# Kernel optimization log

Measured on AMD Instinct MI355X. Metric: run time of the kernel, lower is better.

Reference implementation:

```python
import jax, jax.numpy as jnp
import numpy as np

B, S, D, H, DFF = 2, 2048, 2048, 16, 8192
DH = D // H
EPS = 1e-5


def _layer_norm(x, g, b):
    mu = jnp.mean(x, axis=-1, keepdims=True)
    var = jnp.mean(jnp.square(x - mu), axis=-1, keepdims=True)
    return (x - mu) * jax.lax.rsqrt(var + EPS) * g + b


def setup_inputs() -> dict:
    key = jax.random.key(0)
    ks = jax.random.split(key, 12)
    sc = 0.02
    inp = {
        "x": jax.random.normal(ks[0], (B, S, D), dtype=jnp.float32),
        # attention projections, stored [in, out] (torch Linear weight transposed)
        "wq": jax.random.normal(ks[1], (D, D), dtype=jnp.float32) * sc,
        "bq": jnp.zeros((D,), jnp.float32),
        "wk": jax.random.normal(ks[2], (D, D), dtype=jnp.float32) * sc,
        "bk": jnp.zeros((D,), jnp.float32),
        "wv": jax.random.normal(ks[3], (D, D), dtype=jnp.float32) * sc,
        "bv": jnp.zeros((D,), jnp.float32),
        "wo": jax.random.normal(ks[4], (D, D), dtype=jnp.float32) * sc,
        "bo": jnp.zeros((D,), jnp.float32),
        "ln1_g": jnp.ones((D,), jnp.float32),
        "ln1_b": jnp.zeros((D,), jnp.float32),
        # feed-forward
        "w1": jax.random.normal(ks[5], (D, DFF), dtype=jnp.float32) * sc,
        "b1": jnp.zeros((DFF,), jnp.float32),
        "w2": jax.random.normal(ks[6], (DFF, D), dtype=jnp.float32) * sc,
        "b2": jnp.zeros((D,), jnp.float32),
        "ln2_g": jnp.ones((D,), jnp.float32),
        "ln2_b": jnp.zeros((D,), jnp.float32),
    }
    return inp


def reference(x, wq, bq, wk, bk, wv, bv, wo, bo, ln1_g, ln1_b,
              w1, b1, w2, b2, ln2_g, ln2_b):
    # ---- MultiHeadAttentionBlock: x + MHA(LN(x)) ----
    h = _layer_norm(x, ln1_g, ln1_b)                      # [B,S,D]
    q = (h @ wq + bq).reshape(B, S, H, DH).transpose(0, 2, 1, 3)  # [B,H,S,DH]
    k = (h @ wk + bk).reshape(B, S, H, DH).transpose(0, 2, 1, 3)
    v = (h @ wv + bv).reshape(B, S, H, DH).transpose(0, 2, 1, 3)

    # faithful to source: scale by sqrt(d_dim), NOT sqrt(head_dim)
    scores = jnp.einsum("bhqd,bhkd->bhqk", q, k) / np.sqrt(D).astype(np.float32)
    # faithful triu/transpose masking (softmax sees raw zeros, not -inf)
    t = jnp.triu(scores).swapaxes(-2, -1)                 # [B,H,S,S]
    s = jax.nn.softmax(t, axis=-2)
    r = jnp.triu(s).swapaxes(-2, -1)
    attn = jnp.einsum("bhqk,bhkd->bhqd", r, v)            # [B,H,S,DH]
    attn = attn.transpose(0, 2, 1, 3).reshape(B, S, D)
    x = x + attn @ wo + bo

    # ---- FeedForwardBlock: x + FF(LN(x)), dropout rate 0 ----
    h2 = _layer_norm(x, ln2_g, ln2_b)
    ff = jax.nn.relu(h2 @ w1 + b1) @ w2 + b2
    return x + ff
```

## Files before the change

### kernel.cpp

```cpp
#include <hip/hip_runtime.h>


typedef unsigned short ushort_t;
typedef unsigned int   uint32;
typedef __attribute__((ext_vector_type(8)))  short    short8;
typedef __attribute__((ext_vector_type(8)))  ushort_t ushort8;
typedef __attribute__((ext_vector_type(4)))  float    f32x4;

#define BDIM   2
#define SEQ    2048
#define DMODEL 2048
#define NHEAD  16
#define DHEAD  128
#define DFFN   8192
#define MROWS  (BDIM*SEQ)
#define LDQKV  6144

#define GPTR(p) (const __attribute__((address_space(1))) void*)((const void*)(p))
#define SPTR(p) (__attribute__((address_space(3))) void*)((void*)(p))

__device__ __forceinline__ float bf2f(ushort_t u) {
  union { uint32 i; float f; } c; c.i = ((uint32)u) << 16; return c.f;
}
__device__ __forceinline__ ushort_t f2bf(float f) {
  union { float f; uint32 i; } c; c.f = f;
  uint32 u = c.i;
  return (ushort_t)((u + 0x7fffu + ((u >> 16) & 1u)) >> 16);
}

__global__ __launch_bounds__(256) void prep_kern(
    const float* __restrict__ wq, const float* __restrict__ wk,
    const float* __restrict__ wv, const float* __restrict__ wo,
    const float* __restrict__ w1, const float* __restrict__ w2,
    const float* __restrict__ bq, const float* __restrict__ bk,
    const float* __restrict__ bv,
    ushort_t* __restrict__ WQKV, ushort_t* __restrict__ WOT,
    ushort_t* __restrict__ W1T, ushort_t* __restrict__ W2T,
    float* __restrict__ Bcat)
{
  const int bid = blockIdx.x;
  if (bid >= 49152) {
    for (int i = threadIdx.x; i < 6144; i += 256)
      Bcat[i] = (i < 2048) ? bq[i] : ((i < 4096) ? bk[i - 2048] : bv[i - 4096]);
    return;
  }
  const float* W; ushort_t* Wt; int K, N, local;
  if (bid < 12288) {
    const int which = bid >> 12; local = bid & 4095;
    W = (which == 0) ? wq : (which == 1) ? wk : wv;
    Wt = WQKV + (size_t)which * 2048 * 2048; K = 2048; N = 2048;
  } else if (bid < 16384) { W = wo; Wt = WOT; K = 2048; N = 2048; local = bid - 12288; }
  else if (bid < 32768)   { W = w1; Wt = W1T; K = 2048; N = 8192; local = bid - 16384; }
  else                    { W = w2; Wt = W2T; K = 8192; N = 2048; local = bid - 32768; }
  const int ntiles = N >> 5;
  const int nb = (local % ntiles) * 32, kb = (local / ntiles) * 32;

  __shared__ float tile[32][33];
  const int tx = threadIdx.x & 31, ty = threadIdx.x >> 5;
#pragma unroll
  for (int j = 0; j < 32; j += 8)
    tile[ty + j][tx] = W[(size_t)(kb + ty + j) * N + nb + tx];
  __syncthreads();
#pragma unroll
  for (int j = 0; j < 32; j += 8)
    Wt[(size_t)(nb + ty + j) * K + kb + tx] = f2bf(tile[tx][ty + j]);
}

__global__ __launch_bounds__(256) void ln_kern(
    const float* __restrict__ X, const float* __restrict__ G,
    const float* __restrict__ Bb, ushort_t* __restrict__ Out)
{
  const int row = blockIdx.x, tid = threadIdx.x;
  const float* xr = X + (size_t)row * DMODEL;
  float4 v0 = ((const float4*)xr)[tid * 2];
  float4 v1 = ((const float4*)xr)[tid * 2 + 1];
  float s  = v0.x + v0.y + v0.z + v0.w + v1.x + v1.y + v1.z + v1.w;
  float ss = v0.x*v0.x + v0.y*v0.y + v0.z*v0.z + v0.w*v0.w
           + v1.x*v1.x + v1.y*v1.y + v1.z*v1.z + v1.w*v1.w;
#pragma unroll
  for (int off = 32; off > 0; off >>= 1) {
    s  += __shfl_down(s, off);
    ss += __shfl_down(ss, off);
  }
  __shared__ float rs[4], rss[4];
  __shared__ float sh_mu, sh_rst;
  const int wv = tid >> 6;
  if ((tid & 63) == 0) { rs[wv] = s; rss[wv] = ss; }
  __syncthreads();
  if (tid == 0) {
    float S1 = rs[0] + rs[1] + rs[2] + rs[3];
    float S2 = rss[0] + rss[1] + rss[2] + rss[3];
    float mu = S1 * (1.f / DMODEL);
    float var = S2 * (1.f / DMODEL) - mu * mu;
    sh_mu = mu;
    sh_rst = rsqrtf(var + 1e-5f);
  }
  __syncthreads();
  const float mu = sh_mu, rst = sh_rst;
  float4 g0 = ((const float4*)G)[tid * 2];
  float4 g1 = ((const float4*)G)[tid * 2 + 1];
  float4 b0 = ((const float4*)Bb)[tid * 2];
  float4 b1 = ((const float4*)Bb)[tid * 2 + 1];
  ushort8 o;
  o[0] = f2bf((v0.x - mu) * rst * g0.x + b0.x);
  o[1] = f2bf((v0.y - mu) * rst * g0.y + b0.y);
  o[2] = f2bf((v0.z - mu) * rst * g0.z + b0.z);
  o[3] = f2bf((v0.w - mu) * rst * g0.w + b0.w);
  o[4] = f2bf((v1.x - mu) * rst * g1.x + b1.x);
  o[5] = f2bf((v1.y - mu) * rst * g1.y + b1.y);
  o[6] = f2bf((v1.z - mu) * rst * g1.z + b1.z);
  o[7] = f2bf((v1.w - mu) * rst * g1.w + b1.w);
  *(ushort8*)(Out + (size_t)row * DMODEL + tid * 8) = o;
}

__global__ __launch_bounds__(256) void combine_ln_kern(
    const ushort_t* __restrict__ pp, const float* __restrict__ bias,
    const float* __restrict__ xres, const float* __restrict__ G,
    const float* __restrict__ Bb, float* __restrict__ X2,
    ushort_t* __restrict__ Out)
{
  const int row = blockIdx.x, tid = threadIdx.x;
  const size_t i = (size_t)row * DMODEL + tid * 8;
  ushort8 p0 = *(const ushort8*)(pp + i);
  ushort8 p1 = *(const ushort8*)(pp + (size_t)MROWS * 2048 + i);
  float v[8];
#pragma unroll
  for (int j = 0; j < 8; ++j)
    v[j] = bf2f(p0[j]) + bf2f(p1[j]) + bias[tid * 8 + j] + xres[i + j];
  float4 o0 = {v[0], v[1], v[2], v[3]}, o1 = {v[4], v[5], v[6], v[7]};
  *(float4*)(X2 + i) = o0;
  *(float4*)(X2 + i + 4) = o1;

  float s = 0.f, ss = 0.f;
#pragma unroll
  for (int j = 0; j < 8; ++j) { s += v[j]; ss += v[j] * v[j]; }
#pragma unroll
  for (int off = 32; off > 0; off >>= 1) {
    s  += __shfl_down(s, off);
    ss += __shfl_down(ss, off);
  }
  __shared__ float rs[4], rss[4];
  __shared__ float sh_mu, sh_rst;
  const int wvv = tid >> 6;
  if ((tid & 63) == 0) { rs[wvv] = s; rss[wvv] = ss; }
  __syncthreads();
  if (tid == 0) {
    float S1 = rs[0] + rs[1] + rs[2] + rs[3];
    float S2 = rss[0] + rss[1] + rss[2] + rss[3];
    float mu = S1 * (1.f / DMODEL);
    float var = S2 * (1.f / DMODEL) - mu * mu;
    sh_mu = mu; sh_rst = rsqrtf(var + 1e-5f);
  }
  __syncthreads();
  const float mu = sh_mu, rst = sh_rst;
  ushort8 o;
#pragma unroll
  for (int j = 0; j < 8; ++j)
    o[j] = f2bf((v[j] - mu) * rst * G[tid * 8 + j] + Bb[tid * 8 + j]);
  *(ushort8*)(Out + i) = o;
}

template<int OUT, int RELU, int KDIV>
__global__ __launch_bounds__(512) void gemm_hi_kern(
    const ushort_t* __restrict__ A, const ushort_t* __restrict__ Bt,
    const float* __restrict__ bias, ushort_t* __restrict__ Cout,
    int M, int N, int K)
{
  __shared__ ushort_t sA[3 * 4096];
  __shared__ ushort_t sB[3 * 8192];

  const int tid = threadIdx.x;
  const int nM  = gridDim.y;
  const int nwg = gridDim.x * nM;
  const int bid = blockIdx.y * gridDim.x + blockIdx.x;
  const int cpx = nwg >> 3;
  const int swz = (bid & 7) * cpx + (bid >> 3);
  const int m0 = (swz % nM) * 128;
  const int n0 = (swz / nM) * 256;

  const int Keff = K / KDIV;
  const int k0 = (KDIV > 1) ? blockIdx.z * Keff : 0;
  const int U = Keff >> 5;

  const int l = tid & 63, w = tid >> 6;
  const int lr = l & 15, lg = l >> 4;
  const int wr = w >> 2, wc = w & 3;

  const int xch   = (lg ^ ((lr >> 1) & 3)) * 8;
  const int abase = (wr * 64 + lr) * 32 + xch;
  const int bbase = (wc * 64 + lr) * 32 + xch;

  const int sr = tid >> 2;
  const int sg = ((tid & 3) ^ ((tid >> 3) & 3)) * 8;
  const ushort_t* Asrc = A  + (size_t)(m0 + sr) * K + k0 + sg;
  const ushort_t* Bsrc = Bt + (size_t)(n0 + sr) * K + k0 + sg;
  ushort_t* dA = sA + tid * 8;
  ushort_t* dB = sB + tid * 8;

#define SAU(slot, u) __builtin_amdgcn_global_load_lds( \
    GPTR(Asrc + (size_t)(u) * 32), SPTR(dA + (slot) * 4096), 16, 0, 0)
#define SBU(slot, u, r) __builtin_amdgcn_global_load_lds( \
    GPTR(Bsrc + (size_t)(r) * 128 * K + (size_t)(u) * 32), \
    SPTR(dB + (slot) * 8192 + (r) * 4096), 16, 0, 0)

  f32x4 acc[4][4] = {};

  SAU(0, 0); SBU(0, 0, 0); SBU(0, 0, 1);
  SAU(1, 1); SBU(1, 1, 0); SBU(1, 1, 1);
  asm volatile("s_waitcnt vmcnt(3)" ::: "memory");
  __builtin_amdgcn_s_barrier();

  int cur = 0;
  for (int u = 0; u < U; ++u) {
    const ushort_t* pA = sA + cur * 4096;
    const ushort_t* pB = sB + cur * 8192;
    const int nx = (cur == 0) ? 2 : cur - 1;
    short8 af[4], bf[4];
#pragma unroll
    for (int i = 0; i < 4; ++i) af[i] = *(const short8*)(pA + abase + i * 512);
#pragma unroll
    for (int i = 0; i < 4; ++i) bf[i] = *(const short8*)(pB + bbase + i * 512);
    if (u + 2 < U) { SAU(nx, u + 2); SBU(nx, u + 2, 0); SBU(nx, u + 2, 1); }
    __builtin_amdgcn_s_setprio(1);
#pragma unroll
    for (int mi = 0; mi < 4; ++mi)
#pragma unroll
      for (int ni = 0; ni < 4; ++ni)
        acc[mi][ni] = __builtin_amdgcn_mfma_f32_16x16x32_bf16(
            af[mi], bf[ni], acc[mi][ni], 0, 0, 0);
    __builtin_amdgcn_s_setprio(0);
    if (u < U - 2) { asm volatile("s_waitcnt vmcnt(3)" ::: "memory"); }
    else           { asm volatile("s_waitcnt vmcnt(0)" ::: "memory"); }
    __builtin_amdgcn_s_barrier();
    cur = (cur == 2) ? 0 : cur + 1;
  }
#undef SAU
#undef SBU

  ushort_t* Pz = (OUT == 2)
      ? Cout + (size_t)blockIdx.z * M * N : Cout;
#pragma unroll
  for (int mi = 0; mi < 4; ++mi) {
#pragma unroll
    for (int ni = 0; ni < 4; ++ni) {
      const int gn = n0 + wc * 64 + ni * 16 + lr;
      const float bvv = (OUT == 2) ? 0.f : bias[gn];
#pragma unroll
      for (int j = 0; j < 4; ++j) {
        const int gm = m0 + wr * 64 + mi * 16 + lg * 4 + j;
        float v = acc[mi][ni][j] + bvv;
        if (RELU) v = fmaxf(v, 0.f);
        Pz[(size_t)gm * N + gn] = f2bf(v);
      }
    }
  }
}

__global__ __launch_bounds__(256) void combine_kern(
    const ushort_t* __restrict__ pp, const float* __restrict__ bias,
    const float* __restrict__ resid, float* __restrict__ out)
{
  const size_t i = ((size_t)blockIdx.x * 256 + threadIdx.x) * 8;
  ushort8 p0 = *(const ushort8*)(pp + i);
  ushort8 p1 = *(const ushort8*)(pp + (size_t)MROWS * 2048 + i);
  const int col = (int)(i & 2047);
  float4 r0 = *(const float4*)(resid + i);
  float4 r1 = *(const float4*)(resid + i + 4);
  float4 c0 = *(const float4*)(bias + col);
  float4 c1 = *(const float4*)(bias + col + 4);
  float4 o0, o1;
  o0.x = bf2f(p0[0]) + bf2f(p1[0]) + c0.x + r0.x;
  o0.y = bf2f(p0[1]) + bf2f(p1[1]) + c0.y + r0.y;
  o0.z = bf2f(p0[2]) + bf2f(p1[2]) + c0.z + r0.z;
  o0.w = bf2f(p0[3]) + bf2f(p1[3]) + c0.w + r0.w;
  o1.x = bf2f(p0[4]) + bf2f(p1[4]) + c1.x + r1.x;
  o1.y = bf2f(p0[5]) + bf2f(p1[5]) + c1.y + r1.y;
  o1.z = bf2f(p0[6]) + bf2f(p1[6]) + c1.z + r1.z;
  o1.w = bf2f(p0[7]) + bf2f(p1[7]) + c1.w + r1.w;
  *(float4*)(out + i) = o0;
  *(float4*)(out + i + 4) = o1;
}

__global__ __launch_bounds__(256) void attn_stats_kern(
    const ushort_t* __restrict__ Q, const ushort_t* __restrict__ Kb,
    float* __restrict__ E, float* __restrict__ DG, int ld)
{
  __shared__ ushort_t Ksm[2 * 8192];
  const int qb = blockIdx.x;
  const int bh = blockIdx.y;
  const int b = bh >> 4, h = bh & 15;
  const int tid = threadIdx.x;
  const int l = tid & 63, w = tid >> 6;
  const int lr = l & 15, lg = l >> 4;

  const int qrow0 = qb * 128 + w * 32;

  short8 af[2][4];
#pragma unroll
  for (int g = 0; g < 2; ++g) {
    const size_t qoff = (size_t)(b * SEQ + qrow0 + g * 16 + lr) * ld + h * DHEAD + lg * 8;
#pragma unroll
    for (int c = 0; c < 4; ++c) af[g][c] = *(const short8*)(Q + qoff + c * 32);
  }

  const int srow_b = w * 16 + (l >> 4);
  const ushort_t* Kg = Kb + (size_t)b * SEQ * ld + (size_t)h * DHEAD;

  f32x4 sume[2] = {{0.f,0.f,0.f,0.f},{0.f,0.f,0.f,0.f}};
  f32x4 dge[2]  = {{0.f,0.f,0.f,0.f},{0.f,0.f,0.f,0.f}};
  const float scale = 0.0220970869120796f;
  const int rx = lr & 7;
  const int kc0 = qb * 2;

#define STAGEK(kc, buf) do { \
    _Pragma("unroll") \
    for (int c_ = 0; c_ < 4; ++c_) { \
      const int row_ = srow_b + c_ * 4; \
      const int g_ = (l & 15) ^ (row_ & 7); \
      __builtin_amdgcn_global_load_lds( \
          GPTR(Kg + (size_t)((kc) * 64 + row_) * ld + g_ * 8), \
          SPTR(Ksm + (buf) * 8192 + w * 2048 + c_ * 512), 16, 0, 0); \
    } } while (0)

  STAGEK(kc0, 0);
  __syncthreads();

  int cur = 0;
  for (int kc = kc0; kc < 32; ++kc) {
    if (kc + 1 < 32) STAGEK(kc + 1, cur ^ 1);
    const ushort_t* Kbuf = Ksm + cur * 8192;

    for (int ks = 0; ks < 4; ++ks) {
      const int kbase = kc * 64 + ks * 16;
      if (kbase + 16 <= qrow0) continue;
      short8 bfr[4];
#pragma unroll
      for (int c = 0; c < 4; ++c)
        bfr[c] = *(const short8*)(Kbuf + (ks * 16 + lr) * 128 + ((lg + c * 4) ^ rx) * 8);
#pragma unroll
      for (int g = 0; g < 2; ++g) {
        const int qg = qrow0 + g * 16;
        if (kbase < qg) continue;
        f32x4 sc = {0.f, 0.f, 0.f, 0.f};
        sc = __builtin_amdgcn_mfma_f32_16x16x32_bf16(af[g][0], bfr[0], sc, 0, 0, 0);
        sc = __builtin_amdgcn_mfma_f32_16x16x32_bf16(af[g][1], bfr[1], sc, 0, 0, 0);
        sc = __builtin_amdgcn_mfma_f32_16x16x32_bf16(af[g][2], bfr[2], sc, 0, 0, 0);
        sc = __builtin_amdgcn_mfma_f32_16x16x32_bf16(af[g][3], bfr[3], sc, 0, 0, 0);
        if (kbase == qg) {
          const int ki = kbase + lr;
#pragma unroll
          for (int j = 0; j < 4; ++j) {
            const int qi = qg + lg * 4 + j;
            if (ki >= qi) {
              float e = __expf(sc[j] * scale);
              sume[g][j] += e;
              if (ki == qi) dge[g][j] += e;
            }
          }
        } else {
#pragma unroll
          for (int j = 0; j < 4; ++j)
            sume[g][j] += __expf(sc[j] * scale);
        }
      }
    }
    __syncthreads();
    cur ^= 1;
  }
#undef STAGEK

#pragma unroll
  for (int g = 0; g < 2; ++g) {
#pragma unroll
    for (int j = 0; j < 4; ++j) {
#pragma unroll
      for (int off = 1; off < 16; off <<= 1) {
        sume[g][j] += __shfl_xor(sume[g][j], off);
        dge[g][j]  += __shfl_xor(dge[g][j], off);
      }
    }
  }
  if (lr == 0) {
#pragma unroll
    for (int g = 0; g < 2; ++g)
#pragma unroll
      for (int j = 0; j < 4; ++j) {
        E[(size_t)bh * SEQ + qrow0 + g * 16 + lg * 4 + j]  = sume[g][j];
        DG[(size_t)bh * SEQ + qrow0 + g * 16 + lg * 4 + j] = dge[g][j];
      }
  }
}

__global__ __launch_bounds__(128) void vchunk_kern(
    const ushort_t* __restrict__ V, float* __restrict__ CS, int ld)
{
  const int c = blockIdx.x, bh = blockIdx.y;
  const int b = bh >> 4, h = bh & 15;
  const int dh = threadIdx.x;
  const ushort_t* vp = V + (size_t)(b * SEQ + c * 64) * ld + h * DHEAD + dh;
  float s = 0.f;
  for (int i = 0; i < 64; ++i) s += bf2f(vp[(size_t)i * ld]);
  CS[((size_t)bh * 32 + c) * 128 + dh] = s;
}

__global__ __launch_bounds__(128) void attn_combine_kern(
    const ushort_t* __restrict__ V, const float* __restrict__ CS,
    const float* __restrict__ E, const float* __restrict__ DG,
    ushort_t* __restrict__ Attn, int ldv)
{
  const int c = blockIdx.x, bh = blockIdx.y;
  const int b = bh >> 4, h = bh & 15;
  const int dh = threadIdx.x;
  float prefix = 0.f;
  for (int cc = 0; cc < c; ++cc) prefix += CS[((size_t)bh * 32 + cc) * 128 + dh];
  const ushort_t* vp = V + (size_t)(b * SEQ + c * 64) * ldv + h * DHEAD + dh;
  ushort_t* ap = Attn + (size_t)(b * SEQ + c * 64) * DMODEL + h * DHEAD + dh;
  const int qb = c * 64;
  for (int i = 0; i < 64; ++i) {
    const int qq = qb + i;
    const float denom = (float)qq + E[(size_t)bh * SEQ + qq];
    const float de = DG[(size_t)bh * SEQ + qq];
    const float vv = bf2f(vp[(size_t)i * ldv]);
    ap[(size_t)i * DMODEL] = f2bf((prefix + de * vv) / denom);
    prefix += vv;
  }
}

extern "C" void kernel_launch(void* const* d_in, const int* in_sizes, int n_in,
                              void* d_out, int out_size, void* d_ws, size_t ws_size,
                              hipStream_t stream)
{
  const float* x    = (const float*)d_in[0];
  const float* wq   = (const float*)d_in[1];
  const float* bq   = (const float*)d_in[2];
  const float* wk   = (const float*)d_in[3];
  const float* bk   = (const float*)d_in[4];
  const float* wv   = (const float*)d_in[5];
  const float* bv   = (const float*)d_in[6];
  const float* wo   = (const float*)d_in[7];
  const float* bo   = (const float*)d_in[8];
  const float* ln1g = (const float*)d_in[9];
  const float* ln1b = (const float*)d_in[10];
  const float* w1   = (const float*)d_in[11];
  const float* b1   = (const float*)d_in[12];
  const float* w2   = (const float*)d_in[13];
  const float* b2   = (const float*)d_in[14];
  const float* ln2g = (const float*)d_in[15];
  const float* ln2b = (const float*)d_in[16];
  float* out = (float*)d_out;

  char* ws = (char*)d_ws;
  ushort_t* W1T  = (ushort_t*)(ws + 0);
  ushort_t* PPf2 = (ushort_t*)(ws + 0);
  ushort_t* W2T  = (ushort_t*)(ws + 33554432);
  ushort_t* WOT  = (ushort_t*)(ws + 67108864);
  float*    X2   = (float*)   (ws + 75497472);
  float*    Bcat = (float*)   (ws + 75497472);
  ushort_t* Hb   = (ushort_t*)(ws + 109051904);
  ushort_t* F1   = (ushort_t*)(ws + 125829120);
  ushort_t* PPwo = (ushort_t*)(ws + 125829120);
  ushort_t* WQKV = (ushort_t*)(ws + 125829120);
  ushort_t* QKVb = (ushort_t*)(ws + 150994944);
  float*    Eb   = (float*)   (ws + 201326592);
  float*    DGb  = (float*)   (ws + 201588736);
  float*    CSb  = (float*)   (ws + 201850880);

  prep_kern<<<49153, 256, 0, stream>>>(wq, wk, wv, wo, w1, w2, bq, bk, bv,
                                       WQKV, WOT, W1T, W2T, Bcat);

  ln_kern<<<MROWS, 256, 0, stream>>>(x, ln1g, ln1b, Hb);

  gemm_hi_kern<1, 0, 1><<<dim3(24, 32), 512, 0, stream>>>(
      Hb, WQKV, Bcat, QKVb, MROWS, LDQKV, DMODEL);

  attn_stats_kern<<<dim3(16, 32), 256, 0, stream>>>(QKVb, QKVb + 2048, Eb, DGb, LDQKV);

  vchunk_kern<<<dim3(32, 32), 128, 0, stream>>>(QKVb + 4096, CSb, LDQKV);
  attn_combine_kern<<<dim3(32, 32), 128, 0, stream>>>(QKVb + 4096, CSb, Eb, DGb, Hb, LDQKV);

  gemm_hi_kern<2, 0, 2><<<dim3(8, 32, 2), 512, 0, stream>>>(
      Hb, WOT, bo, PPwo, MROWS, DMODEL, DMODEL);

  combine_ln_kern<<<MROWS, 256, 0, stream>>>(PPwo, bo, x, ln2g, ln2b, X2, Hb);

  gemm_hi_kern<1, 1, 1><<<dim3(32, 32), 512, 0, stream>>>(
      Hb, W1T, b1, F1, MROWS, DFFN, DMODEL);

  gemm_hi_kern<2, 0, 2><<<dim3(8, 32, 2), 512, 0, stream>>>(
      F1, W2T, b2, PPf2, MROWS, DMODEL, DFFN);
  combine_kern<<<4096, 256, 0, stream>>>(PPf2, b2, X2, out);
}
```

Measured before the change: 619.9 us.

## Drop split-K for output GEMMs and fuse bias plus residual into epilogue

The Wo and W2 projections no longer use split-K with bf16 partial buffers followed by separate combine kernels. The GEMM epilogue now adds bias and the fp32 residual and writes fp32 output directly, and the second LayerNorm reuses the plain ln_kern on X2. This removes two extra kernels, the partial-sum traffic, and a bf16 rounding of the partials. In exchange those GEMMs launch only 256 workgroups instead of 512, which lowers occupancy on a large-CU GPU, and the epilogue issues scattered 4-byte fp32 stores.

```diff
diff --git a/kernel.cpp b/kernel.cpp
--- a/kernel.cpp
+++ b/kernel.cpp
@@ -113,58 +113,11 @@
   *(ushort8*)(Out + (size_t)row * DMODEL + tid * 8) = o;
 }
 
-__global__ __launch_bounds__(256) void combine_ln_kern(
-    const ushort_t* __restrict__ pp, const float* __restrict__ bias,
-    const float* __restrict__ xres, const float* __restrict__ G,
-    const float* __restrict__ Bb, float* __restrict__ X2,
-    ushort_t* __restrict__ Out)
-{
-  const int row = blockIdx.x, tid = threadIdx.x;
-  const size_t i = (size_t)row * DMODEL + tid * 8;
-  ushort8 p0 = *(const ushort8*)(pp + i);
-  ushort8 p1 = *(const ushort8*)(pp + (size_t)MROWS * 2048 + i);
-  float v[8];
-#pragma unroll
-  for (int j = 0; j < 8; ++j)
-    v[j] = bf2f(p0[j]) + bf2f(p1[j]) + bias[tid * 8 + j] + xres[i + j];
-  float4 o0 = {v[0], v[1], v[2], v[3]}, o1 = {v[4], v[5], v[6], v[7]};
-  *(float4*)(X2 + i) = o0;
-  *(float4*)(X2 + i + 4) = o1;
-
-  float s = 0.f, ss = 0.f;
-#pragma unroll
-  for (int j = 0; j < 8; ++j) { s += v[j]; ss += v[j] * v[j]; }
-#pragma unroll
-  for (int off = 32; off > 0; off >>= 1) {
-    s  += __shfl_down(s, off);
-    ss += __shfl_down(ss, off);
-  }
-  __shared__ float rs[4], rss[4];
-  __shared__ float sh_mu, sh_rst;
-  const int wvv = tid >> 6;
-  if ((tid & 63) == 0) { rs[wvv] = s; rss[wvv] = ss; }
-  __syncthreads();
-  if (tid == 0) {
-    float S1 = rs[0] + rs[1] + rs[2] + rs[3];
-    float S2 = rss[0] + rss[1] + rss[2] + rss[3];
-    float mu = S1 * (1.f / DMODEL);
-    float var = S2 * (1.f / DMODEL) - mu * mu;
-    sh_mu = mu; sh_rst = rsqrtf(var + 1e-5f);
-  }
-  __syncthreads();
-  const float mu = sh_mu, rst = sh_rst;
-  ushort8 o;
-#pragma unroll
-  for (int j = 0; j < 8; ++j)
-    o[j] = f2bf((v[j] - mu) * rst * G[tid * 8 + j] + Bb[tid * 8 + j]);
-  *(ushort8*)(Out + i) = o;
-}
-
-template<int OUT, int RELU, int KDIV>
+template<int OUT, int RELU>
 __global__ __launch_bounds__(512) void gemm_hi_kern(
     const ushort_t* __restrict__ A, const ushort_t* __restrict__ Bt,
-    const float* __restrict__ bias, ushort_t* __restrict__ Cout,
-    int M, int N, int K)
+    const float* __restrict__ bias, const float* __restrict__ resid,
+    void* __restrict__ Cout, int M, int N, int K)
 {
   __shared__ ushort_t sA[3 * 4096];
   __shared__ ushort_t sB[3 * 8192];
@@ -178,9 +131,7 @@
   const int m0 = (swz % nM) * 128;
   const int n0 = (swz / nM) * 256;
 
-  const int Keff = K / KDIV;
-  const int k0 = (KDIV > 1) ? blockIdx.z * Keff : 0;
-  const int U = Keff >> 5;
+  const int U = K >> 5;
 
   const int l = tid & 63, w = tid >> 6;
   const int lr = l & 15, lg = l >> 4;
@@ -192,8 +143,8 @@
 
   const int sr = tid >> 2;
   const int sg = ((tid & 3) ^ ((tid >> 3) & 3)) * 8;
-  const ushort_t* Asrc = A  + (size_t)(m0 + sr) * K + k0 + sg;
-  const ushort_t* Bsrc = Bt + (size_t)(n0 + sr) * K + k0 + sg;
+  const ushort_t* Asrc = A  + (size_t)(m0 + sr) * K + sg;
+  const ushort_t* Bsrc = Bt + (size_t)(n0 + sr) * K + sg;
   ushort_t* dA = sA + tid * 8;
   ushort_t* dB = sB + tid * 8;
 
@@ -237,48 +188,26 @@
 #undef SAU
 #undef SBU
 
-  ushort_t* Pz = (OUT == 2)
-      ? Cout + (size_t)blockIdx.z * M * N : Cout;
 #pragma unroll
   for (int mi = 0; mi < 4; ++mi) {
 #pragma unroll
     for (int ni = 0; ni < 4; ++ni) {
       const int gn = n0 + wc * 64 + ni * 16 + lr;
-      const float bvv = (OUT == 2) ? 0.f : bias[gn];
+      const float bvv = bias[gn];
 #pragma unroll
       for (int j = 0; j < 4; ++j) {
         const int gm = m0 + wr * 64 + mi * 16 + lg * 4 + j;
         float v = acc[mi][ni][j] + bvv;
-        if (RELU) v = fmaxf(v, 0.f);
-        Pz[(size_t)gm * N + gn] = f2bf(v);
+        if (OUT == 0) {
+          v += resid[(size_t)gm * N + gn];
+          ((float*)Cout)[(size_t)gm * N + gn] = v;
+        } else {
+          if (RELU) v = fmaxf(v, 0.f);
+          ((ushort_t*)Cout)[(size_t)gm * N + gn] = f2bf(v);
+        }
       }
     }
   }
-}
-
-__global__ __launch_bounds__(256) void combine_kern(
-    const ushort_t* __restrict__ pp, const float* __restrict__ bias,
-    const float* __restrict__ resid, float* __restrict__ out)
-{
-  const size_t i = ((size_t)blockIdx.x * 256 + threadIdx.x) * 8;
-  ushort8 p0 = *(const ushort8*)(pp + i);
-  ushort8 p1 = *(const ushort8*)(pp + (size_t)MROWS * 2048 + i);
-  const int col = (int)(i & 2047);
-  float4 r0 = *(const float4*)(resid + i);
-  float4 r1 = *(const float4*)(resid + i + 4);
-  float4 c0 = *(const float4*)(bias + col);
-  float4 c1 = *(const float4*)(bias + col + 4);
-  float4 o0, o1;
-  o0.x = bf2f(p0[0]) + bf2f(p1[0]) + c0.x + r0.x;
-  o0.y = bf2f(p0[1]) + bf2f(p1[1]) + c0.y + r0.y;
-  o0.z = bf2f(p0[2]) + bf2f(p1[2]) + c0.z + r0.z;
-  o0.w = bf2f(p0[3]) + bf2f(p1[3]) + c0.w + r0.w;
-  o1.x = bf2f(p0[4]) + bf2f(p1[4]) + c1.x + r1.x;
-  o1.y = bf2f(p0[5]) + bf2f(p1[5]) + c1.y + r1.y;
-  o1.z = bf2f(p0[6]) + bf2f(p1[6]) + c1.z + r1.z;
-  o1.w = bf2f(p0[7]) + bf2f(p1[7]) + c1.w + r1.w;
-  *(float4*)(out + i) = o0;
-  *(float4*)(out + i + 4) = o1;
 }
 
 __global__ __launch_bounds__(256) void attn_stats_kern(
@@ -451,14 +380,12 @@
 
   char* ws = (char*)d_ws;
   ushort_t* W1T  = (ushort_t*)(ws + 0);
-  ushort_t* PPf2 = (ushort_t*)(ws + 0);
   ushort_t* W2T  = (ushort_t*)(ws + 33554432);
   ushort_t* WOT  = (ushort_t*)(ws + 67108864);
   float*    X2   = (float*)   (ws + 75497472);
   float*    Bcat = (float*)   (ws + 75497472);
   ushort_t* Hb   = (ushort_t*)(ws + 109051904);
   ushort_t* F1   = (ushort_t*)(ws + 125829120);
-  ushort_t* PPwo = (ushort_t*)(ws + 125829120);
   ushort_t* WQKV = (ushort_t*)(ws + 125829120);
   ushort_t* QKVb = (ushort_t*)(ws + 150994944);
   float*    Eb   = (float*)   (ws + 201326592);
@@ -470,23 +397,22 @@
 
   ln_kern<<<MROWS, 256, 0, stream>>>(x, ln1g, ln1b, Hb);
 
-  gemm_hi_kern<1, 0, 1><<<dim3(24, 32), 512, 0, stream>>>(
-      Hb, WQKV, Bcat, QKVb, MROWS, LDQKV, DMODEL);
+  gemm_hi_kern<1, 0><<<dim3(24, 32), 512, 0, stream>>>(
+      Hb, WQKV, Bcat, nullptr, QKVb, MROWS, LDQKV, DMODEL);
 
   attn_stats_kern<<<dim3(16, 32), 256, 0, stream>>>(QKVb, QKVb + 2048, Eb, DGb, LDQKV);
 
   vchunk_kern<<<dim3(32, 32), 128, 0, stream>>>(QKVb + 4096, CSb, LDQKV);
   attn_combine_kern<<<dim3(32, 32), 128, 0, stream>>>(QKVb + 4096, CSb, Eb, DGb, Hb, LDQKV);
 
-  gemm_hi_kern<2, 0, 2><<<dim3(8, 32, 2), 512, 0, stream>>>(
-      Hb, WOT, bo, PPwo, MROWS, DMODEL, DMODEL);
-
-  combine_ln_kern<<<MROWS, 256, 0, stream>>>(PPwo, bo, x, ln2g, ln2b, X2, Hb);
-
-  gemm_hi_kern<1, 1, 1><<<dim3(32, 32), 512, 0, stream>>>(
-      Hb, W1T, b1, F1, MROWS, DFFN, DMODEL);
-
-  gemm_hi_kern<2, 0, 2><<<dim3(8, 32, 2), 512, 0, stream>>>(
-      F1, W2T, b2, PPf2, MROWS, DMODEL, DFFN);
-  combine_kern<<<4096, 256, 0, stream>>>(PPf2, b2, X2, out);
-}
+  gemm_hi_kern<0, 0><<<dim3(8, 32), 512, 0, stream>>>(
+      Hb, WOT, bo, x, X2, MROWS, DMODEL, DMODEL);
+
+  ln_kern<<<MROWS, 256, 0, stream>>>(X2, ln2g, ln2b, Hb);
+
+  gemm_hi_kern<1, 1><<<dim3(32, 32), 512, 0, stream>>>(
+      Hb, W1T, b1, nullptr, F1, MROWS, DFFN, DMODEL);
+
+  gemm_hi_kern<0, 0><<<dim3(8, 32), 512, 0, stream>>>(
+      F1, W2T, b2, X2, out, MROWS, DMODEL, DFFN);
+}
```

Measured after the change: 636.9 us. +2.7%, slower.
